# Performance work log

Hardware: AMD Instinct MI355X
Metric: run time of the kernel (lower is better)

Reference implementation:

```python
import jax, jax.numpy as jnp
import numpy as np

# dims
B, T = 2, 256            # batch, seq_len
V, H_CP, R = 512, 2, 2   # vocab, CP horizon, CP rank
E, L, NH, NPOS = 768, 12, 12, 1024  # n_embd, n_layer, n_head, max positions
HD = E // NH             # head dim = 64


def _ln(x, g, b, eps=1e-5):
    m = jnp.mean(x, -1, keepdims=True)
    v = jnp.mean((x - m) ** 2, -1, keepdims=True)
    return (x - m) * jax.lax.rsqrt(v + eps) * g + b


def setup_inputs() -> dict:
    key = jax.random.key(0)
    ks = jax.random.split(key, 10)
    s = 0.02  # GPT2 init std
    n = lambda k, sh: s * jax.random.normal(k, sh, jnp.float32)
    return {
        "input_ids": jax.random.randint(ks[0], (B, T), 0, V, dtype=jnp.int32),
        "wte": n(ks[1], (V, E)),
        "wpe": n(ks[2], (NPOS, E)),
        "ln1_g": jnp.ones((L, E), jnp.float32), "ln1_b": jnp.zeros((L, E), jnp.float32),
        "ln2_g": jnp.ones((L, E), jnp.float32), "ln2_b": jnp.zeros((L, E), jnp.float32),
        "w_qkv": n(ks[3], (L, E, 3 * E)), "b_qkv": jnp.zeros((L, 3 * E), jnp.float32),
        "w_ao": n(ks[4], (L, E, E)), "b_ao": jnp.zeros((L, E), jnp.float32),
        "w_fc": n(ks[5], (L, E, 4 * E)), "b_fc": jnp.zeros((L, 4 * E), jnp.float32),
        "w_mo": n(ks[6], (L, 4 * E, E)), "b_mo": jnp.zeros((L, E), jnp.float32),
        "lnf_g": jnp.ones((E,), jnp.float32), "lnf_b": jnp.zeros((E,), jnp.float32),
        "w_cp": n(ks[7], (E, H_CP * V * R)), "b_cp": jnp.zeros((H_CP * V * R,), jnp.float32),
    }


def reference(input_ids, wte, wpe, ln1_g, ln1_b, ln2_g, ln2_b, w_qkv, b_qkv,
              w_ao, b_ao, w_fc, b_fc, w_mo, b_mo, lnf_g, lnf_b, w_cp, b_cp):
    # --- GPT2 transformer body (eval mode: dropout inactive) ---
    h = wte[input_ids] + wpe[:T]                      # (B,T,E)
    causal = jnp.tril(jnp.ones((T, T), bool))
    inv_sqrt_hd = float(1.0 / np.sqrt(HD))

    def block(h, p):
        l1g, l1b, l2g, l2b, wq, bq, wa, ba, wf, bf, wm, bm = p
        x = _ln(h, l1g, l1b)
        qkv = x @ wq + bq                             # (B,T,3E)
        q, k, v = jnp.split(qkv, 3, axis=-1)
        q = q.reshape(B, T, NH, HD).transpose(0, 2, 1, 3)
        k = k.reshape(B, T, NH, HD).transpose(0, 2, 1, 3)
        v = v.reshape(B, T, NH, HD).transpose(0, 2, 1, 3)
        att = jnp.einsum('bhqd,bhkd->bhqk', q, k) * inv_sqrt_hd
        att = jnp.where(causal, att, jnp.float32(-1e9))
        att = jax.nn.softmax(att, axis=-1)
        o = jnp.einsum('bhqk,bhkd->bhqd', att, v).transpose(0, 2, 1, 3).reshape(B, T, E)
        h = h + o @ wa + ba
        x = _ln(h, l2g, l2b)
        h = h + jax.nn.gelu(x @ wf + bf, approximate=True) @ wm + bm  # gelu_new
        return h, None

    h, _ = jax.lax.scan(block, h, (ln1_g, ln1_b, ln2_g, ln2_b, w_qkv, b_qkv,
                                   w_ao, b_ao, w_fc, b_fc, w_mo, b_mo))
    h = _ln(h, lnf_g, lnf_b)                          # last_hidden_state

    # --- CP joint distribution: sum_r outer(f0_r, f1_r), then positivity(exp) ---
    cp = (h.reshape(B * T, E) @ w_cp + b_cp).reshape(B * T, H_CP, V, R)
    scores = jnp.einsum('nir,njr->nij', cp[:, 0], cp[:, 1])  # (B*T, V, V)
    mjd = jnp.exp(scores).reshape(B, T, V, V)[:, :-H_CP].reshape(-1, V, V)

    # --- windowed targets: targets[b,t,h] = input_ids[b, t+1+h] ---
    off = jnp.arange(T - H_CP)[:, None] + 1 + jnp.arange(H_CP)[None, :]
    tgt = input_ids[:, off].reshape(-1, H_CP)         # (B*(T-H), H)

    # --- entropy loss over unnormalized joint: mean(log Z - log p_target) ---
    n = mjd.shape[0]
    p_t = mjd[jnp.arange(n), tgt[:, 0], tgt[:, 1]]
    Z = mjd.sum((1, 2))
    loss = jnp.mean(jnp.log(Z) - jnp.log(p_t))
    return loss
```

## Files before the change

### kernel.cpp

```cpp
#include <hip/hip_runtime.h>

typedef unsigned short u16;
typedef short short8 __attribute__((ext_vector_type(8)));
typedef float f32x4 __attribute__((ext_vector_type(4)));

constexpr int B_  = 2;
constexpr int T_  = 256;
constexpr int V_  = 512;
constexpr int E_  = 768;
constexpr int L_  = 12;
constexpr int NH_ = 12;
constexpr int HD_ = 64;
constexpr int E3_ = 3 * E_;
constexpr int E4_ = 4 * E_;
constexpr int CPD_ = 2048;
constexpr int NTOK_ = B_ * T_;
constexpr int NVALID_ = B_ * (T_ - 2);
constexpr size_t PS_ = (size_t)NTOK_ * E_;
constexpr size_t QS_ = (size_t)NTOK_ * E3_;
constexpr size_t FS_ = (size_t)NTOK_ * E4_;
constexpr size_t CS_ = (size_t)NTOK_ * CPD_;

__device__ __forceinline__ u16 f2b(float f) {
    union { float f; unsigned int u; } c; c.f = f;
    unsigned int r = (c.u + 0x7FFFu + ((c.u >> 16) & 1u)) >> 16; return (u16)r;
}

__global__ __launch_bounds__(256) void ln_res_k(float* __restrict__ h,
    const float* __restrict__ pb, int np,
    const int* __restrict__ ids, const float* __restrict__ wte,
    const float* __restrict__ wpe,
    const float* __restrict__ g, const float* __restrict__ bta,
    u16* __restrict__ out) {
    int n = blockIdx.x;
    int tid = threadIdx.x;
    size_t off = (size_t)n * E_;
    float v0, v1, v2;
    if (np < 0) {
        int t = n % T_;
        int tok = ids[n];
        size_t wo = (size_t)tok * E_, po = (size_t)t * E_;
        v0 = wte[wo + tid]       + wpe[po + tid];
        v1 = wte[wo + tid + 256] + wpe[po + tid + 256];
        v2 = wte[wo + tid + 512] + wpe[po + tid + 512];
        h[off + tid] = v0; h[off + tid + 256] = v1; h[off + tid + 512] = v2;
    } else {
        v0 = h[off + tid]; v1 = h[off + tid + 256]; v2 = h[off + tid + 512];
        for (int j = 0; j < np; j++) {
            const float* p = pb + (size_t)j * PS_ + off;
            v0 += p[tid]; v1 += p[tid + 256]; v2 += p[tid + 512];
        }
        if (np) { h[off + tid] = v0; h[off + tid + 256] = v1; h[off + tid + 512] = v2; }
    }
    __shared__ float red[256];
    red[tid] = v0 + v1 + v2;
    __syncthreads();
    for (int o = 128; o > 0; o >>= 1) { if (tid < o) red[tid] += red[tid + o]; __syncthreads(); }
    float mean = red[0] * (1.0f / E_);
    __syncthreads();
    float d0 = v0 - mean, d1 = v1 - mean, d2 = v2 - mean;
    red[tid] = d0 * d0 + d1 * d1 + d2 * d2;
    __syncthreads();
    for (int o = 128; o > 0; o >>= 1) { if (tid < o) red[tid] += red[tid + o]; __syncthreads(); }
    float rstd = rsqrtf(red[0] * (1.0f / E_) + 1e-5f);
    u16* y = out + off;
    y[tid]       = f2b(d0 * rstd * g[tid]       + bta[tid]);
    y[tid + 256] = f2b(d1 * rstd * g[tid + 256] + bta[tid + 256]);
    y[tid + 512] = f2b(d2 * rstd * g[tid + 512] + bta[tid + 512]);
}

__global__ __launch_bounds__(512) void mgemm_k(const u16* __restrict__ A,
    const float* __restrict__ W, const float* __restrict__ bias,
    float* __restrict__ outP, int K, int KC, int N) {
    __shared__ u16 As[128 * 40];
    __shared__ u16 Bs[128 * 40];
    int tid = threadIdx.x, lane = tid & 63, wid = tid >> 6;
    int ln15 = lane & 15, quad = lane >> 4;
    int col0 = blockIdx.x * 128, row0 = blockIdx.y * 128;
    int kz = blockIdx.z, kbase = kz * KC;
    int ar = tid >> 2, ak = (tid & 3) * 8;
    const u16* Ag = A + (size_t)(row0 + ar) * K + kbase + ak;
    u16* Aw = &As[ar * 40 + ak];
    int bc = tid & 127, kg = (tid >> 7) * 8;
    const float* Wg = W + (size_t)(kbase + kg) * N + col0 + bc;
    u16* Bw = &Bs[bc * 40 + kg];
    int wr = (wid & 3) * 32, wc = (wid >> 2) * 64;

    f32x4 acc[2][4];
#pragma unroll
    for (int mt = 0; mt < 2; mt++)
#pragma unroll
        for (int nt = 0; nt < 4; nt++) acc[mt][nt] = (f32x4){0.f, 0.f, 0.f, 0.f};

    uint4 av = *(const uint4*)Ag;
    float w[8];
#pragma unroll
    for (int i = 0; i < 8; i++) w[i] = Wg[(size_t)i * N];

    for (int k0 = 0; k0 < KC; k0 += 32) {
        uint4 avn = av;
        float wn[8];
#pragma unroll
        for (int i = 0; i < 8; i++) wn[i] = w[i];
        if (k0 + 32 < KC) {
            avn = *(const uint4*)(Ag + k0 + 32);
#pragma unroll
            for (int i = 0; i < 8; i++) wn[i] = Wg[(size_t)(k0 + 32 + i) * N];
        }
        uint4 bv;
        asm("v_cvt_pk_bf16_f32 %0, %1, %2" : "=v"(bv.x) : "v"(w[0]), "v"(w[1]));
        asm("v_cvt_pk_bf16_f32 %0, %1, %2" : "=v"(bv.y) : "v"(w[2]), "v"(w[3]));
        asm("v_cvt_pk_bf16_f32 %0, %1, %2" : "=v"(bv.z) : "v"(w[4]), "v"(w[5]));
        asm("v_cvt_pk_bf16_f32 %0, %1, %2" : "=v"(bv.w) : "v"(w[6]), "v"(w[7]));
        __syncthreads();
        *(uint4*)Aw = av;
        *(uint4*)Bw = bv;
        __syncthreads();
        short8 af[2], bf[4];
#pragma unroll
        for (int mt = 0; mt < 2; mt++)
            af[mt] = *(const short8*)&As[(wr + mt * 16 + ln15) * 40 + quad * 8];
#pragma unroll
        for (int nt = 0; nt < 4; nt++)
            bf[nt] = *(const short8*)&Bs[(wc + nt * 16 + ln15) * 40 + quad * 8];
#pragma unroll
        for (int mt = 0; mt < 2; mt++)
#pragma unroll
            for (int nt = 0; nt < 4; nt++)
                acc[mt][nt] = __builtin_amdgcn_mfma_f32_16x16x32_bf16(
                    af[mt], bf[nt], acc[mt][nt], 0, 0, 0);
        av = avn;
#pragma unroll
        for (int i = 0; i < 8; i++) w[i] = wn[i];
    }
    float* dst = outP + (size_t)kz * NTOK_ * N;
#pragma unroll
    for (int mt = 0; mt < 2; mt++) {
#pragma unroll
        for (int nt = 0; nt < 4; nt++) {
            int c = col0 + wc + nt * 16 + ln15;
            float bb = (kz == 0) ? bias[c] : 0.f;
#pragma unroll
            for (int r = 0; r < 4; r++) {
                int rw = row0 + wr + mt * 16 + quad * 4 + r;
                dst[(size_t)rw * N + c] = acc[mt][nt][r] + bb;
            }
        }
    }
}

__global__ __launch_bounds__(256) void gelu_k(const float* __restrict__ p0,
    const float* __restrict__ p1, u16* __restrict__ out) {
    size_t i = ((size_t)blockIdx.x * 256 + threadIdx.x) * 4;
    float4 a = *(const float4*)&p0[i];
    float4 b = *(const float4*)&p1[i];
    float u[4] = {a.x + b.x, a.y + b.y, a.z + b.z, a.w + b.w};
    ushort4 o;
    u16* op = (u16*)&o;
#pragma unroll
    for (int j = 0; j < 4; j++) {
        float uu = u[j];
        float inner = 0.7978845608028654f * (uu + 0.044715f * uu * uu * uu);
        op[j] = f2b(0.5f * uu * (1.0f + tanhf(inner)));
    }
    *(ushort4*)&out[i] = o;
}

constexpr int KSTR_ = 72;
constexpr int PSTR_ = 264;
__global__ __launch_bounds__(256) void fattn_k(const float* __restrict__ qp,
    u16* __restrict__ o) {
    __shared__ u16 Ks[256 * KSTR_];
    __shared__ u16 Vt[64 * PSTR_];
    __shared__ u16 Ps[64 * PSTR_];
    int qt = blockIdx.x;
    int bh = blockIdx.y;
    int hh = bh % NH_, b = bh / NH_;
    int tid = threadIdx.x, lane = tid & 63, wid = tid >> 6;
    int ln15 = lane & 15, quad = lane >> 4;

    int sr = tid >> 4, sd = (tid & 15) * 4;
#pragma unroll
    for (int pass = 0; pass < 16; pass++) {
        int rr = sr + pass * 16;
        size_t rowbase = (size_t)(b * T_ + rr) * E3_ + hh * HD_ + sd;
        float kx = 0.f, ky = 0.f, kz = 0.f, kw = 0.f;
        float vx = 0.f, vy = 0.f, vz = 0.f, vw = 0.f;
#pragma unroll
        for (int pi = 0; pi < 4; pi++) {
            float4 kk = *(const float4*)&qp[pi * QS_ + rowbase + E_];
            float4 vv = *(const float4*)&qp[pi * QS_ + rowbase + 2 * E_];
            kx += kk.x; ky += kk.y; kz += kk.z; kw += kk.w;
            vx += vv.x; vy += vv.y; vz += vv.z; vw += vv.w;
        }
        uint2 pk;
        asm("v_cvt_pk_bf16_f32 %0, %1, %2" : "=v"(pk.x) : "v"(kx), "v"(ky));
        asm("v_cvt_pk_bf16_f32 %0, %1, %2" : "=v"(pk.y) : "v"(kz), "v"(kw));
        *(uint2*)&Ks[rr * KSTR_ + sd] = pk;
        Vt[(sd + 0) * PSTR_ + rr] = f2b(vx);
        Vt[(sd + 1) * PSTR_ + rr] = f2b(vy);
        Vt[(sd + 2) * PSTR_ + rr] = f2b(vz);
        Vt[(sd + 3) * PSTR_ + rr] = f2b(vw);
    }

    size_t qbase = (size_t)(b * T_ + qt * 64 + wid * 16 + ln15) * E3_ + hh * HD_;
    short8 qf[2];
#pragma unroll
    for (int ks = 0; ks < 2; ks++) {
        float s8[8] = {0.f, 0.f, 0.f, 0.f, 0.f, 0.f, 0.f, 0.f};
#pragma unroll
        for (int pi = 0; pi < 4; pi++) {
            const float* src = &qp[pi * QS_ + qbase + ks * 32 + quad * 8];
            float4 a = *(const float4*)src;
            float4 b4 = *(const float4*)(src + 4);
            s8[0] += a.x; s8[1] += a.y; s8[2] += a.z; s8[3] += a.w;
            s8[4] += b4.x; s8[5] += b4.y; s8[6] += b4.z; s8[7] += b4.w;
        }
        union { short8 s; unsigned int u[4]; } uq;
#pragma unroll
        for (int i = 0; i < 4; i++)
            asm("v_cvt_pk_bf16_f32 %0, %1, %2" : "=v"(uq.u[i]) : "v"(s8[2 * i]), "v"(s8[2 * i + 1]));
        qf[ks] = uq.s;
    }

    __syncthreads();

    f32x4 s[16];
#pragma unroll
    for (int nt = 0; nt < 16; nt++) s[nt] = (f32x4){0.f, 0.f, 0.f, 0.f};
#pragma unroll
    for (int ks = 0; ks < 2; ks++) {
#pragma unroll
        for (int nt = 0; nt < 16; nt++) {
            short8 kf = *(const short8*)&Ks[(nt * 16 + ln15) * KSTR_ + ks * 32 + quad * 8];
            s[nt] = __builtin_amdgcn_mfma_f32_16x16x32_bf16(qf[ks], kf, s[nt], 0, 0, 0);
        }
    }

#pragma unroll
    for (int r = 0; r < 4; r++) {
        int q = qt * 64 + wid * 16 + quad * 4 + r;
        float m = -1e30f;
#pragma unroll
        for (int nt = 0; nt < 16; nt++) {
            int j = nt * 16 + ln15;
            float sv = (j <= q) ? s[nt][r] * 0.125f : -1e9f;
            s[nt][r] = sv;
            m = fmaxf(m, sv);
        }
        m = fmaxf(m, __shfl_xor(m, 1));
        m = fmaxf(m, __shfl_xor(m, 2));
        m = fmaxf(m, __shfl_xor(m, 4));
        m = fmaxf(m, __shfl_xor(m, 8));
        float sum = 0.f;
#pragma unroll
        for (int nt = 0; nt < 16; nt++) {
            float p = __expf(s[nt][r] - m);
            s[nt][r] = p;
            sum += p;
        }
        sum += __shfl_xor(sum, 1);
        sum += __shfl_xor(sum, 2);
        sum += __shfl_xor(sum, 4);
        sum += __shfl_xor(sum, 8);
        float inv = 1.0f / sum;
#pragma unroll
        for (int nt = 0; nt < 16; nt++) s[nt][r] *= inv;
    }

#pragma unroll
    for (int nt = 0; nt < 16; nt++)
#pragma unroll
        for (int r = 0; r < 4; r++)
            Ps[(wid * 16 + quad * 4 + r) * PSTR_ + nt * 16 + ln15] = f2b(s[nt][r]);

    __syncthreads();

    f32x4 oacc[4];
#pragma unroll
    for (int dt = 0; dt < 4; dt++) oacc[dt] = (f32x4){0.f, 0.f, 0.f, 0.f};
#pragma unroll
    for (int ks = 0; ks < 8; ks++) {
        short8 pf = *(const short8*)&Ps[(wid * 16 + ln15) * PSTR_ + ks * 32 + quad * 8];
#pragma unroll
        for (int dt = 0; dt < 4; dt++) {
            short8 vf = *(const short8*)&Vt[(dt * 16 + ln15) * PSTR_ + ks * 32 + quad * 8];
            oacc[dt] = __builtin_amdgcn_mfma_f32_16x16x32_bf16(pf, vf, oacc[dt], 0, 0, 0);
        }
    }

#pragma unroll
    for (int dt = 0; dt < 4; dt++) {
#pragma unroll
        for (int r = 0; r < 4; r++) {
            int q = qt * 64 + wid * 16 + quad * 4 + r;
            o[(size_t)(b * T_ + q) * E_ + hh * HD_ + dt * 16 + ln15] = f2b(oacc[dt][r]);
        }
    }
}

__global__ __launch_bounds__(256) void zloss_k(const float* __restrict__ cp,
    const int* __restrict__ ids, float* __restrict__ lossv) {
    int n = blockIdx.x;
    int b = n / (T_ - 2), t = n % (T_ - 2);
    int nf = b * T_ + t;
    size_t base = (size_t)nf * CPD_;
    __shared__ float A0[V_], A1[V_], B0[V_], B1[V_];
    __shared__ float red[256];
    int tid = threadIdx.x;
    for (int v = tid; v < V_; v += 256) {
        float a0 = 0.f, a1 = 0.f, b0 = 0.f, b1 = 0.f;
#pragma unroll
        for (int pi = 0; pi < 4; pi++) {
            const float* ap = cp + pi * CS_ + base;
            float2 av = *(const float2*)&ap[2 * v];
            float2 bv = *(const float2*)&ap[1024 + 2 * v];
            a0 += av.x; a1 += av.y; b0 += bv.x; b1 += bv.y;
        }
        A0[v] = a0; A1[v] = a1; B0[v] = b0; B1[v] = b1;
    }
    __syncthreads();
    float acc = 0.f;
    for (int j = tid; j < V_; j += 256) {
        float b0 = B0[j], b1 = B1[j];
        for (int i = 0; i < V_; i++)
            acc += __expf(A0[i] * b0 + A1[i] * b1);
    }
    red[tid] = acc; __syncthreads();
    for (int off = 128; off > 0; off >>= 1) { if (tid < off) red[tid] += red[tid + off]; __syncthreads(); }
    if (tid == 0) {
        int t0 = ids[b * T_ + t + 1];
        int t1 = ids[b * T_ + t + 2];
        float score = A0[t0] * B0[t1] + A1[t0] * B1[t1];
        lossv[n] = logf(red[0]) - score;
    }
}

__global__ __launch_bounds__(256) void reduce_k(const float* __restrict__ lossv,
    unsigned int* __restrict__ out) {
    __shared__ float red[256];
    int tid = threadIdx.x;
    float s = 0.f;
    for (int i = tid; i < NVALID_; i += 256) s += lossv[i];
    red[tid] = s; __syncthreads();
    for (int off = 128; off > 0; off >>= 1) { if (tid < off) red[tid] += red[tid + off]; __syncthreads(); }
    if (tid == 0) {
        float loss = red[0] / (float)NVALID_;
        union { float f; unsigned int u; } cv; cv.f = loss;
        unsigned int b = (cv.u + 0x7FFFu + ((cv.u >> 16) & 1u)) >> 16;
        out[0] = (b << 16) | b;
    }
}

extern "C" void kernel_launch(void* const* d_in, const int* in_sizes, int n_in,
                              void* d_out, int out_size, void* d_ws, size_t ws_size,
                              hipStream_t stream) {
    const int*   ids  = (const int*)d_in[0];
    const float* wte  = (const float*)d_in[1];
    const float* wpe  = (const float*)d_in[2];
    const float* ln1g = (const float*)d_in[3];
    const float* ln1b = (const float*)d_in[4];
    const float* ln2g = (const float*)d_in[5];
    const float* ln2b = (const float*)d_in[6];
    const float* wqkv = (const float*)d_in[7];
    const float* bqkv = (const float*)d_in[8];
    const float* wao  = (const float*)d_in[9];
    const float* bao  = (const float*)d_in[10];
    const float* wfc  = (const float*)d_in[11];
    const float* bfc  = (const float*)d_in[12];
    const float* wmo  = (const float*)d_in[13];
    const float* bmo  = (const float*)d_in[14];
    const float* lnfg = (const float*)d_in[15];
    const float* lnfb = (const float*)d_in[16];
    const float* wcp  = (const float*)d_in[17];
    const float* bcp  = (const float*)d_in[18];

    char* p = (char*)d_ws;
    float* h    = (float*)p; p += (size_t)NTOK_ * E_ * 4;
    u16*   x    = (u16*)p;   p += (size_t)NTOK_ * E_ * 2;
    u16*   aob  = (u16*)p;   p += (size_t)NTOK_ * E_ * 2;
    u16*   fcb  = (u16*)p;   p += (size_t)NTOK_ * E4_ * 2;
    float* pbuf = (float*)p; p += 4 * QS_ * 4;
    float* lossv = (float*)p; p += 4096;

    for (int l = 0; l < L_; l++) {
        ln_res_k<<<NTOK_, 256, 0, stream>>>(h, pbuf, l ? 8 : -1, ids, wte, wpe,
                                            ln1g + l * E_, ln1b + l * E_, x);
        mgemm_k<<<dim3(E3_ / 128, 4, 4), 512, 0, stream>>>(
            x, wqkv + (size_t)l * E_ * E3_, bqkv + l * E3_, pbuf, E_, 192, E3_);
        fattn_k<<<dim3(4, B_ * NH_), 256, 0, stream>>>(pbuf, aob);
        mgemm_k<<<dim3(E_ / 128, 4, 8), 512, 0, stream>>>(
            aob, wao + (size_t)l * E_ * E_, bao + l * E_, pbuf, E_, 96, E_);
        ln_res_k<<<NTOK_, 256, 0, stream>>>(h, pbuf, 8, ids, wte, wpe,
                                            ln2g + l * E_, ln2b + l * E_, x);
        mgemm_k<<<dim3(E4_ / 128, 4, 2), 512, 0, stream>>>(
            x, wfc + (size_t)l * E_ * E4_, bfc + l * E4_, pbuf, E_, 384, E4_);
        gelu_k<<<(NTOK_ * E4_) / 1024, 256, 0, stream>>>(pbuf, pbuf + FS_, fcb);
        mgemm_k<<<dim3(E_ / 128, 4, 8), 512, 0, stream>>>(
            fcb, wmo + (size_t)l * E4_ * E_, bmo + l * E_, pbuf, E4_, 384, E_);
    }
    ln_res_k<<<NTOK_, 256, 0, stream>>>(h, pbuf, 8, ids, wte, wpe, lnfg, lnfb, x);
    mgemm_k<<<dim3(CPD_ / 128, 4, 4), 512, 0, stream>>>(
        x, wcp, bcp, pbuf, E_, 192, CPD_);
    zloss_k<<<NVALID_, 256, 0, stream>>>(pbuf, ids, lossv);
    reduce_k<<<1, 256, 0, stream>>>(lossv, (unsigned int*)d_out);
}
```

Measured before the change: 1.321 ms.

## Fuse whole forward pass into one cooperative persistent megakernel with grid syncs

After: 4.523 ms. +242.3%, slower.

```diff
diff --git a/kernel.cpp b/kernel.cpp
--- a/kernel.cpp
+++ b/kernel.cpp
@@ -1,4 +1,7 @@
 #include <hip/hip_runtime.h>
+#include <hip/hip_cooperative_groups.h>
+
+namespace cg = cooperative_groups;
 
 typedef unsigned short u16;
 typedef short short8 __attribute__((ext_vector_type(8)));
@@ -25,6 +28,7 @@
     union { float f; unsigned int u; } c; c.f = f;
     unsigned int r = (c.u + 0x7FFFu + ((c.u >> 16) & 1u)) >> 16; return (u16)r;
 }
+
 
 __global__ __launch_bounds__(256) void ln_res_k(float* __restrict__ h,
     const float* __restrict__ pb, int np,
@@ -352,6 +356,406 @@
     }
 }
 
+
+struct MKP {
+    const int* ids; const float* wte; const float* wpe;
+    const float* ln1g; const float* ln1b; const float* ln2g; const float* ln2b;
+    const float* wqkv; const float* bqkv; const float* wao; const float* bao;
+    const float* wfc; const float* bfc; const float* wmo; const float* bmo;
+    const float* lnfg; const float* lnfb; const float* wcp; const float* bcp;
+    float* h; u16* x; u16* aob; u16* fcb; float* pbuf; float* lossv;
+    unsigned int* out;
+};
+
+__device__ void mk_ln_unit(int n, float* h, const float* pb, int np,
+    const int* ids, const float* wte, const float* wpe,
+    const float* g, const float* bta, u16* out, float* red) {
+    int tid = threadIdx.x;
+    size_t off = (size_t)n * E_;
+    float v0 = 0.f, v1 = 0.f, v2 = 0.f;
+    if (tid < 256) {
+        if (np < 0) {
+            int t = n % T_;
+            int tok = ids[n];
+            size_t wo = (size_t)tok * E_, po = (size_t)t * E_;
+            v0 = wte[wo + tid]       + wpe[po + tid];
+            v1 = wte[wo + tid + 256] + wpe[po + tid + 256];
+            v2 = wte[wo + tid + 512] + wpe[po + tid + 512];
+            h[off + tid] = v0; h[off + tid + 256] = v1; h[off + tid + 512] = v2;
+        } else {
+            v0 = h[off + tid]; v1 = h[off + tid + 256]; v2 = h[off + tid + 512];
+            for (int j = 0; j < np; j++) {
+                const float* p = pb + (size_t)j * PS_ + off;
+                v0 += p[tid]; v1 += p[tid + 256]; v2 += p[tid + 512];
+            }
+            if (np) { h[off + tid] = v0; h[off + tid + 256] = v1; h[off + tid + 512] = v2; }
+        }
+        red[tid] = v0 + v1 + v2;
+    }
+    __syncthreads();
+    for (int o = 128; o > 0; o >>= 1) { if (tid < o) red[tid] += red[tid + o]; __syncthreads(); }
+    float mean = red[0] * (1.0f / E_);
+    __syncthreads();
+    float d0 = v0 - mean, d1 = v1 - mean, d2 = v2 - mean;
+    if (tid < 256) red[tid] = d0 * d0 + d1 * d1 + d2 * d2;
+    __syncthreads();
+    for (int o = 128; o > 0; o >>= 1) { if (tid < o) red[tid] += red[tid + o]; __syncthreads(); }
+    float rstd = rsqrtf(red[0] * (1.0f / E_) + 1e-5f);
+    if (tid < 256) {
+        u16* y = out + off;
+        y[tid]       = f2b(d0 * rstd * g[tid]       + bta[tid]);
+        y[tid + 256] = f2b(d1 * rstd * g[tid + 256] + bta[tid + 256]);
+        y[tid + 512] = f2b(d2 * rstd * g[tid + 512] + bta[tid + 512]);
+    }
+    __syncthreads();
+}
+
+__device__ void mk_gemm(const u16* __restrict__ A, const float* __restrict__ W,
+    const float* __restrict__ bias, float* __restrict__ outP,
+    int K, int KC, int N, int ntiles, int nx, u16* As, u16* Bs) {
+    int tid = threadIdx.x, lane = tid & 63, wid = tid >> 6;
+    int ln15 = lane & 15, quad = lane >> 4;
+    int ar = tid >> 2, ak = (tid & 3) * 8;
+    int bc = tid & 127, kg = (tid >> 7) * 8;
+    int wr = (wid & 3) * 32, wc = (wid >> 2) * 64;
+    for (int t = blockIdx.x; t < ntiles; t += 256) {
+        int bx = t % nx, by = (t / nx) & 3, kz = t / (nx * 4);
+        int col0 = bx * 128, row0 = by * 128, kbase = kz * KC;
+        const u16* Ag = A + (size_t)(row0 + ar) * K + kbase + ak;
+        u16* Aw = &As[ar * 40 + ak];
+        const float* Wg = W + (size_t)(kbase + kg) * N + col0 + bc;
+        u16* Bw = &Bs[bc * 40 + kg];
+
+        f32x4 acc[2][4];
+#pragma unroll
+        for (int mt = 0; mt < 2; mt++)
+#pragma unroll
+            for (int nt = 0; nt < 4; nt++) acc[mt][nt] = (f32x4){0.f, 0.f, 0.f, 0.f};
+
+        uint4 av = *(const uint4*)Ag;
+        float w[8];
+#pragma unroll
+        for (int i = 0; i < 8; i++) w[i] = Wg[(size_t)i * N];
+
+        for (int k0 = 0; k0 < KC; k0 += 32) {
+            uint4 avn = av;
+            float wn[8];
+#pragma unroll
+            for (int i = 0; i < 8; i++) wn[i] = w[i];
+            if (k0 + 32 < KC) {
+                avn = *(const uint4*)(Ag + k0 + 32);
+#pragma unroll
+                for (int i = 0; i < 8; i++) wn[i] = Wg[(size_t)(k0 + 32 + i) * N];
+            }
+            uint4 bv;
+            asm("v_cvt_pk_bf16_f32 %0, %1, %2" : "=v"(bv.x) : "v"(w[0]), "v"(w[1]));
+            asm("v_cvt_pk_bf16_f32 %0, %1, %2" : "=v"(bv.y) : "v"(w[2]), "v"(w[3]));
+            asm("v_cvt_pk_bf16_f32 %0, %1, %2" : "=v"(bv.z) : "v"(w[4]), "v"(w[5]));
+            asm("v_cvt_pk_bf16_f32 %0, %1, %2" : "=v"(bv.w) : "v"(w[6]), "v"(w[7]));
+            __syncthreads();
+            *(uint4*)Aw = av;
+            *(uint4*)Bw = bv;
+            __syncthreads();
+            short8 af[2], bf[4];
+#pragma unroll
+            for (int mt = 0; mt < 2; mt++)
+                af[mt] = *(const short8*)&As[(wr + mt * 16 + ln15) * 40 + quad * 8];
+#pragma unroll
+            for (int nt = 0; nt < 4; nt++)
+                bf[nt] = *(const short8*)&Bs[(wc + nt * 16 + ln15) * 40 + quad * 8];
+#pragma unroll
+            for (int mt = 0; mt < 2; mt++)
+#pragma unroll
+                for (int nt = 0; nt < 4; nt++)
+                    acc[mt][nt] = __builtin_amdgcn_mfma_f32_16x16x32_bf16(
+                        af[mt], bf[nt], acc[mt][nt], 0, 0, 0);
+            av = avn;
+#pragma unroll
+            for (int i = 0; i < 8; i++) w[i] = wn[i];
+        }
+        float* dst = outP + (size_t)kz * NTOK_ * N;
+#pragma unroll
+        for (int mt = 0; mt < 2; mt++) {
+#pragma unroll
+            for (int nt = 0; nt < 4; nt++) {
+                int c = col0 + wc + nt * 16 + ln15;
+                float bb = (kz == 0) ? bias[c] : 0.f;
+#pragma unroll
+                for (int r = 0; r < 4; r++) {
+                    int rw = row0 + wr + mt * 16 + quad * 4 + r;
+                    dst[(size_t)rw * N + c] = acc[mt][nt][r] + bb;
+                }
+            }
+        }
+        __syncthreads();
+    }
+}
+
+__device__ void mk_attn_unit(const float* __restrict__ qp, u16* __restrict__ o,
+    int unit, u16* Ks, u16* Vt, u16* Ps) {
+    int qt = unit % 4, bh = unit / 4;
+    int hh = bh % NH_, b = bh / NH_;
+    int tid = threadIdx.x, lane = tid & 63, wid = tid >> 6;
+    int ln15 = lane & 15, quad = lane >> 4;
+
+    int sr = tid >> 4, sd = (tid & 15) * 4;
+#pragma unroll
+    for (int pass = 0; pass < 8; pass++) {
+        int rr = sr + pass * 32;
+        size_t rowbase = (size_t)(b * T_ + rr) * E3_ + hh * HD_ + sd;
+        float kx = 0.f, ky = 0.f, kz = 0.f, kw = 0.f;
+        float vx = 0.f, vy = 0.f, vz = 0.f, vw = 0.f;
+#pragma unroll
+        for (int pi = 0; pi < 4; pi++) {
+            float4 kk = *(const float4*)&qp[pi * QS_ + rowbase + E_];
+            float4 vv = *(const float4*)&qp[pi * QS_ + rowbase + 2 * E_];
+            kx += kk.x; ky += kk.y; kz += kk.z; kw += kk.w;
+            vx += vv.x; vy += vv.y; vz += vv.z; vw += vv.w;
+        }
+        uint2 pk;
+        asm("v_cvt_pk_bf16_f32 %0, %1, %2" : "=v"(pk.x) : "v"(kx), "v"(ky));
+        asm("v_cvt_pk_bf16_f32 %0, %1, %2" : "=v"(pk.y) : "v"(kz), "v"(kw));
+        *(uint2*)&Ks[rr * KSTR_ + sd] = pk;
+        Vt[(sd + 0) * PSTR_ + rr] = f2b(vx);
+        Vt[(sd + 1) * PSTR_ + rr] = f2b(vy);
+        Vt[(sd + 2) * PSTR_ + rr] = f2b(vz);
+        Vt[(sd + 3) * PSTR_ + rr] = f2b(vw);
+    }
+
+    short8 qf[2];
+    f32x4 s[16];
+    if (tid < 256) {
+        size_t qbase = (size_t)(b * T_ + qt * 64 + wid * 16 + ln15) * E3_ + hh * HD_;
+#pragma unroll
+        for (int ks = 0; ks < 2; ks++) {
+            float s8[8] = {0.f, 0.f, 0.f, 0.f, 0.f, 0.f, 0.f, 0.f};
+#pragma unroll
+            for (int pi = 0; pi < 4; pi++) {
+                const float* src = &qp[pi * QS_ + qbase + ks * 32 + quad * 8];
+                float4 a = *(const float4*)src;
+                float4 b4 = *(const float4*)(src + 4);
+                s8[0] += a.x; s8[1] += a.y; s8[2] += a.z; s8[3] += a.w;
+                s8[4] += b4.x; s8[5] += b4.y; s8[6] += b4.z; s8[7] += b4.w;
+            }
+            union { short8 s; unsigned int u[4]; } uq;
+#pragma unroll
+            for (int i = 0; i < 4; i++)
+                asm("v_cvt_pk_bf16_f32 %0, %1, %2" : "=v"(uq.u[i]) : "v"(s8[2 * i]), "v"(s8[2 * i + 1]));
+            qf[ks] = uq.s;
+        }
+    }
+
+    __syncthreads();
+
+    if (tid < 256) {
+#pragma unroll
+        for (int nt = 0; nt < 16; nt++) s[nt] = (f32x4){0.f, 0.f, 0.f, 0.f};
+#pragma unroll
+        for (int ks = 0; ks < 2; ks++) {
+#pragma unroll
+            for (int nt = 0; nt < 16; nt++) {
+                short8 kf = *(const short8*)&Ks[(nt * 16 + ln15) * KSTR_ + ks * 32 + quad * 8];
+                s[nt] = __builtin_amdgcn_mfma_f32_16x16x32_bf16(qf[ks], kf, s[nt], 0, 0, 0);
+            }
+        }
+#pragma unroll
+        for (int r = 0; r < 4; r++) {
+            int q = qt * 64 + wid * 16 + quad * 4 + r;
+            float m = -1e30f;
+#pragma unroll
+            for (int nt = 0; nt < 16; nt++) {
+                int j = nt * 16 + ln15;
+                float sv = (j <= q) ? s[nt][r] * 0.125f : -1e9f;
+                s[nt][r] = sv;
+                m = fmaxf(m, sv);
+            }
+            m = fmaxf(m, __shfl_xor(m, 1));
+            m = fmaxf(m, __shfl_xor(m, 2));
+            m = fmaxf(m, __shfl_xor(m, 4));
+            m = fmaxf(m, __shfl_xor(m, 8));
+            float sum = 0.f;
+#pragma unroll
+            for (int nt = 0; nt < 16; nt++) {
+                float p = __expf(s[nt][r] - m);
+                s[nt][r] = p;
+                sum += p;
+            }
+            sum += __shfl_xor(sum, 1);
+            sum += __shfl_xor(sum, 2);
+            sum += __shfl_xor(sum, 4);
+            sum += __shfl_xor(sum, 8);
+            float inv = 1.0f / sum;
+#pragma unroll
+            for (int nt = 0; nt < 16; nt++) s[nt][r] *= inv;
+        }
+    }
+
+    __syncthreads();
+
+    if (tid < 256) {
+#pragma unroll
+        for (int nt = 0; nt < 16; nt++)
+#pragma unroll
+            for (int r = 0; r < 4; r++)
+                Ps[(wid * 16 + quad * 4 + r) * PSTR_ + nt * 16 + ln15] = f2b(s[nt][r]);
+    }
+
+    __syncthreads();
+
+    if (tid < 256) {
+        f32x4 oacc[4];
+#pragma unroll
+        for (int dt = 0; dt < 4; dt++) oacc[dt] = (f32x4){0.f, 0.f, 0.f, 0.f};
+#pragma unroll
+        for (int ks = 0; ks < 8; ks++) {
+            short8 pf = *(const short8*)&Ps[(wid * 16 + ln15) * PSTR_ + ks * 32 + quad * 8];
+#pragma unroll
+            for (int dt = 0; dt < 4; dt++) {
+                short8 vf = *(const short8*)&Vt[(dt * 16 + ln15) * PSTR_ + ks * 32 + quad * 8];
+                oacc[dt] = __builtin_amdgcn_mfma_f32_16x16x32_bf16(pf, vf, oacc[dt], 0, 0, 0);
+            }
+        }
+#pragma unroll
+        for (int dt = 0; dt < 4; dt++) {
+#pragma unroll
+            for (int r = 0; r < 4; r++) {
+                int q = qt * 64 + wid * 16 + quad * 4 + r;
+                o[(size_t)(b * T_ + q) * E_ + hh * HD_ + dt * 16 + ln15] = f2b(oacc[dt][r]);
+            }
+        }
+    }
+}
+
+__device__ void mk_zloss_unit(const float* cp, const int* ids, float* lossv, int n,
+    float* A0, float* A1, float* B0, float* B1, float* red) {
+    int b = n / (T_ - 2), t = n % (T_ - 2);
+    int nf = b * T_ + t;
+    size_t base = (size_t)nf * CPD_;
+    int tid = threadIdx.x;
+    if (tid < 256) {
+        for (int v = tid; v < V_; v += 256) {
+            float a0 = 0.f, a1 = 0.f, b0 = 0.f, b1 = 0.f;
+#pragma unroll
+            for (int pi = 0; pi < 4; pi++) {
+                const float* ap = cp + pi * CS_ + base;
+                float2 av = *(const float2*)&ap[2 * v];
+                float2 bv = *(const float2*)&ap[1024 + 2 * v];
+                a0 += av.x; a1 += av.y; b0 += bv.x; b1 += bv.y;
+            }
+            A0[v] = a0; A1[v] = a1; B0[v] = b0; B1[v] = b1;
+        }
+    }
+    __syncthreads();
+    float acc = 0.f;
+    if (tid < 256) {
+        for (int j = tid; j < V_; j += 256) {
+            float b0 = B0[j], b1 = B1[j];
+            for (int i = 0; i < V_; i++)
+                acc += __expf(A0[i] * b0 + A1[i] * b1);
+        }
+        red[tid] = acc;
+    }
+    __syncthreads();
+    for (int off = 128; off > 0; off >>= 1) { if (tid < off) red[tid] += red[tid + off]; __syncthreads(); }
+    if (tid == 0) {
+        int t0 = ids[b * T_ + t + 1];
+        int t1 = ids[b * T_ + t + 2];
+        float score = A0[t0] * B0[t1] + A1[t0] * B1[t1];
+        lossv[n] = logf(red[0]) - score;
+    }
+    __syncthreads();
+}
+
+__device__ void mk_reduce(const float* lossv, unsigned int* out, float* red) {
+    int tid = threadIdx.x;
+    if (tid < 256) {
+        float s = 0.f;
+        for (int i = tid; i < NVALID_; i += 256) s += lossv[i];
+        red[tid] = s;
+    }
+    __syncthreads();
+    for (int off = 128; off > 0; off >>= 1) { if (tid < off) red[tid] += red[tid + off]; __syncthreads(); }
+    if (tid == 0) {
+        float loss = red[0] / (float)NVALID_;
+        union { float f; unsigned int u; } cv; cv.f = loss;
+        unsigned int b = (cv.u + 0x7FFFu + ((cv.u >> 16) & 1u)) >> 16;
+        out[0] = (b << 16) | b;
+    }
+}
+
+__global__ __launch_bounds__(512, 2) void mega_k(MKP p) {
+    cg::grid_group grid = cg::this_grid();
+    __shared__ __align__(16) unsigned char smem[70656];
+    u16* As = (u16*)smem;
+    u16* Bs = (u16*)(smem + 10240);
+    u16* Ks = (u16*)smem;
+    u16* Vt = (u16*)(smem + 36864);
+    u16* Ps = Ks;
+    float* red = (float*)smem;
+    float* zA0 = (float*)smem;
+    float* zA1 = zA0 + 512;
+    float* zB0 = zA0 + 1024;
+    float* zB1 = zA0 + 1536;
+    float* zred = zA0 + 2048;
+    int blk = blockIdx.x;
+
+    for (int l = 0; l < L_; l++) {
+        for (int u = blk; u < NTOK_; u += 256)
+            mk_ln_unit(u, p.h, p.pbuf, l ? 8 : -1, p.ids, p.wte, p.wpe,
+                       p.ln1g + l * E_, p.ln1b + l * E_, p.x, red);
+        grid.sync();
+        mk_gemm(p.x, p.wqkv + (size_t)l * E_ * E3_, p.bqkv + l * E3_, p.pbuf,
+                E_, 192, E3_, 288, 18, As, Bs);
+        grid.sync();
+        if (blk < 96) mk_attn_unit(p.pbuf, p.aob, blk, Ks, Vt, Ps);
+        grid.sync();
+        mk_gemm(p.aob, p.wao + (size_t)l * E_ * E_, p.bao + l * E_, p.pbuf,
+                E_, 96, E_, 192, 6, As, Bs);
+        grid.sync();
+        for (int u = blk; u < NTOK_; u += 256)
+            mk_ln_unit(u, p.h, p.pbuf, 8, p.ids, p.wte, p.wpe,
+                       p.ln2g + l * E_, p.ln2b + l * E_, p.x, red);
+        grid.sync();
+        mk_gemm(p.x, p.wfc + (size_t)l * E_ * E4_, p.bfc + l * E4_, p.pbuf,
+                E_, 384, E4_, 192, 24, As, Bs);
+        grid.sync();
+        {
+            const float* p0 = p.pbuf;
+            const float* p1 = p.pbuf + FS_;
+            size_t nitems = (size_t)NTOK_ * E4_ / 4;
+            for (size_t it = (size_t)blk * 512 + threadIdx.x; it < nitems; it += (size_t)256 * 512) {
+                size_t i = it * 4;
+                float4 a = *(const float4*)&p0[i];
+                float4 b = *(const float4*)&p1[i];
+                float u4[4] = {a.x + b.x, a.y + b.y, a.z + b.z, a.w + b.w};
+                ushort4 o;
+                u16* op = (u16*)&o;
+#pragma unroll
+                for (int j = 0; j < 4; j++) {
+                    float uu = u4[j];
+                    float inner = 0.7978845608028654f * (uu + 0.044715f * uu * uu * uu);
+                    op[j] = f2b(0.5f * uu * (1.0f + tanhf(inner)));
+                }
+                *(ushort4*)&p.fcb[i] = o;
+            }
+        }
+        grid.sync();
+        mk_gemm(p.fcb, p.wmo + (size_t)l * E4_ * E_, p.bmo + l * E_, p.pbuf,
+                E4_, 384, E_, 192, 6, As, Bs);
+        grid.sync();
+    }
+    for (int u = blk; u < NTOK_; u += 256)
+        mk_ln_unit(u, p.h, p.pbuf, 8, p.ids, p.wte, p.wpe, p.lnfg, p.lnfb, p.x, red);
+    grid.sync();
+    mk_gemm(p.x, p.wcp, p.bcp, p.pbuf, E_, 192, CPD_, 256, 16, As, Bs);
+    grid.sync();
+    for (int u = blk; u < NVALID_; u += 256)
+        mk_zloss_unit(p.pbuf, p.ids, p.lossv, u, zA0, zA1, zB0, zB1, zred);
+    grid.sync();
+    if (blk == 0) mk_reduce(p.lossv, p.out, red);
+}
+
+
 extern "C" void kernel_launch(void* const* d_in, const int* in_sizes, int n_in,
                               void* d_out, int out_size, void* d_ws, size_t ws_size,
                               hipStream_t stream) {
@@ -383,6 +787,21 @@
     float* pbuf = (float*)p; p += 4 * QS_ * 4;
     float* lossv = (float*)p; p += 4096;
 
+    MKP mk;
+    mk.ids = ids; mk.wte = wte; mk.wpe = wpe;
+    mk.ln1g = ln1g; mk.ln1b = ln1b; mk.ln2g = ln2g; mk.ln2b = ln2b;
+    mk.wqkv = wqkv; mk.bqkv = bqkv; mk.wao = wao; mk.bao = bao;
+    mk.wfc = wfc; mk.bfc = bfc; mk.wmo = wmo; mk.bmo = bmo;
+    mk.lnfg = lnfg; mk.lnfb = lnfb; mk.wcp = wcp; mk.bcp = bcp;
+    mk.h = h; mk.x = x; mk.aob = aob; mk.fcb = fcb; mk.pbuf = pbuf;
+    mk.lossv = lossv; mk.out = (unsigned int*)d_out;
+
+    void* kargs[] = { (void*)&mk };
+    hipError_t err = hipLaunchCooperativeKernel((const void*)mega_k,
+        dim3(256), dim3(512), kargs, 0, stream);
+    if (err == hipSuccess) return;
+    (void)hipGetLastError();
+
     for (int l = 0; l < L_; l++) {
         ln_res_k<<<NTOK_, 256, 0, stream>>>(h, pbuf, l ? 8 : -1, ids, wte, wpe,
                                             ln1g + l * E_, ln1b + l * E_, x);
```

## Replace split-K QKV/FC GEMMs with full-K bf16-output GEMM fusing bias and GELU

Applied to the files above, without the earlier changes.

After: 1.235 ms, median of 2. 6.5% less time.

```diff
diff --git a/kernel.cpp b/kernel.cpp
--- a/kernel.cpp
+++ b/kernel.cpp
@@ -18,7 +18,6 @@
 constexpr int NVALID_ = B_ * (T_ - 2);
 constexpr size_t PS_ = (size_t)NTOK_ * E_;
 constexpr size_t QS_ = (size_t)NTOK_ * E3_;
-constexpr size_t FS_ = (size_t)NTOK_ * E4_;
 constexpr size_t CS_ = (size_t)NTOK_ * CPD_;
 
 __device__ __forceinline__ u16 f2b(float f) {
@@ -149,26 +148,94 @@
     }
 }
 
-__global__ __launch_bounds__(256) void gelu_k(const float* __restrict__ p0,
-    const float* __restrict__ p1, u16* __restrict__ out) {
-    size_t i = ((size_t)blockIdx.x * 256 + threadIdx.x) * 4;
-    float4 a = *(const float4*)&p0[i];
-    float4 b = *(const float4*)&p1[i];
-    float u[4] = {a.x + b.x, a.y + b.y, a.z + b.z, a.w + b.w};
-    ushort4 o;
-    u16* op = (u16*)&o;
-#pragma unroll
-    for (int j = 0; j < 4; j++) {
-        float uu = u[j];
-        float inner = 0.7978845608028654f * (uu + 0.044715f * uu * uu * uu);
-        op[j] = f2b(0.5f * uu * (1.0f + tanhf(inner)));
-    }
-    *(ushort4*)&out[i] = o;
+__global__ __launch_bounds__(512) void mgemm64_k(const u16* __restrict__ A,
+    const float* __restrict__ W, const float* __restrict__ bias,
+    u16* __restrict__ outB, int K, int N, int mode) {
+    __shared__ u16 As[128 * 40];
+    __shared__ u16 Bs[64 * 40];
+    int tid = threadIdx.x, lane = tid & 63, wid = tid >> 6;
+    int ln15 = lane & 15, quad = lane >> 4;
+    int col0 = blockIdx.x * 64, row0 = blockIdx.y * 128;
+    int ar = tid >> 2, ak = (tid & 3) * 8;
+    const u16* Ag = A + (size_t)(row0 + ar) * K + ak;
+    u16* Aw = &As[ar * 40 + ak];
+    int bc = tid & 63, kg = (tid >> 6) * 4;
+    const float* Wg = W + (size_t)kg * N + col0 + bc;
+    u16* Bw = &Bs[bc * 40 + kg];
+    int wr = (wid & 3) * 32, wc = (wid >> 2) * 32;
+
+    f32x4 acc[2][2];
+    acc[0][0] = (f32x4){0.f,0.f,0.f,0.f}; acc[0][1] = (f32x4){0.f,0.f,0.f,0.f};
+    acc[1][0] = (f32x4){0.f,0.f,0.f,0.f}; acc[1][1] = (f32x4){0.f,0.f,0.f,0.f};
+
+    uint4 av = *(const uint4*)Ag;
+    float w[4];
+#pragma unroll
+    for (int i = 0; i < 4; i++) w[i] = Wg[(size_t)i * N];
+
+    for (int k0 = 0; k0 < K; k0 += 32) {
+        uint4 avn = av;
+        float wn[4];
+#pragma unroll
+        for (int i = 0; i < 4; i++) wn[i] = w[i];
+        if (k0 + 32 < K) {
+            avn = *(const uint4*)(Ag + k0 + 32);
+#pragma unroll
+            for (int i = 0; i < 4; i++) wn[i] = Wg[(size_t)(k0 + 32 + i) * N];
+        }
+        uint2 bv;
+        asm("v_cvt_pk_bf16_f32 %0, %1, %2" : "=v"(bv.x) : "v"(w[0]), "v"(w[1]));
+        asm("v_cvt_pk_bf16_f32 %0, %1, %2" : "=v"(bv.y) : "v"(w[2]), "v"(w[3]));
+        __syncthreads();
+        *(uint4*)Aw = av;
+        *(uint2*)Bw = bv;
+        __syncthreads();
+        short8 af[2], bf[2];
+#pragma unroll
+        for (int mt = 0; mt < 2; mt++)
+            af[mt] = *(const short8*)&As[(wr + mt * 16 + ln15) * 40 + quad * 8];
+#pragma unroll
+        for (int nt = 0; nt < 2; nt++)
+            bf[nt] = *(const short8*)&Bs[(wc + nt * 16 + ln15) * 40 + quad * 8];
+#pragma unroll
+        for (int mt = 0; mt < 2; mt++)
+#pragma unroll
+            for (int nt = 0; nt < 2; nt++)
+                acc[mt][nt] = __builtin_amdgcn_mfma_f32_16x16x32_bf16(
+                    af[mt], bf[nt], acc[mt][nt], 0, 0, 0);
+        av = avn;
+#pragma unroll
+        for (int i = 0; i < 4; i++) w[i] = wn[i];
+    }
+#pragma unroll
+    for (int mt = 0; mt < 2; mt++) {
+#pragma unroll
+        for (int nt = 0; nt < 2; nt++) {
+            int c = col0 + wc + nt * 16 + ln15;
+            float bb = bias[c];
+            if (mode == 3) {
+#pragma unroll
+                for (int r = 0; r < 4; r++) {
+                    int rw = row0 + wr + mt * 16 + quad * 4 + r;
+                    outB[(size_t)rw * N + c] = f2b(acc[mt][nt][r] + bb);
+                }
+            } else {
+#pragma unroll
+                for (int r = 0; r < 4; r++) {
+                    int rw = row0 + wr + mt * 16 + quad * 4 + r;
+                    float u = acc[mt][nt][r] + bb;
+                    float inner = 0.7978845608028654f * (u + 0.044715f * u * u * u);
+                    float v = 0.5f * u * (1.0f + tanhf(inner));
+                    outB[(size_t)rw * N + c] = f2b(v);
+                }
+            }
+        }
+    }
 }
 
 constexpr int KSTR_ = 72;
 constexpr int PSTR_ = 264;
-__global__ __launch_bounds__(256) void fattn_k(const float* __restrict__ qp,
+__global__ __launch_bounds__(256) void fattn_k(const u16* __restrict__ qkv,
     u16* __restrict__ o) {
     __shared__ u16 Ks[256 * KSTR_];
     __shared__ u16 Vt[64 * PSTR_];
@@ -183,45 +250,20 @@
 #pragma unroll
     for (int pass = 0; pass < 16; pass++) {
         int rr = sr + pass * 16;
-        size_t rowbase = (size_t)(b * T_ + rr) * E3_ + hh * HD_ + sd;
-        float kx = 0.f, ky = 0.f, kz = 0.f, kw = 0.f;
-        float vx = 0.f, vy = 0.f, vz = 0.f, vw = 0.f;
-#pragma unroll
-        for (int pi = 0; pi < 4; pi++) {
-            float4 kk = *(const float4*)&qp[pi * QS_ + rowbase + E_];
-            float4 vv = *(const float4*)&qp[pi * QS_ + rowbase + 2 * E_];
-            kx += kk.x; ky += kk.y; kz += kk.z; kw += kk.w;
-            vx += vv.x; vy += vv.y; vz += vv.z; vw += vv.w;
-        }
-        uint2 pk;
-        asm("v_cvt_pk_bf16_f32 %0, %1, %2" : "=v"(pk.x) : "v"(kx), "v"(ky));
-        asm("v_cvt_pk_bf16_f32 %0, %1, %2" : "=v"(pk.y) : "v"(kz), "v"(kw));
-        *(uint2*)&Ks[rr * KSTR_ + sd] = pk;
-        Vt[(sd + 0) * PSTR_ + rr] = f2b(vx);
-        Vt[(sd + 1) * PSTR_ + rr] = f2b(vy);
-        Vt[(sd + 2) * PSTR_ + rr] = f2b(vz);
-        Vt[(sd + 3) * PSTR_ + rr] = f2b(vw);
-    }
-
-    size_t qbase = (size_t)(b * T_ + qt * 64 + wid * 16 + ln15) * E3_ + hh * HD_;
+        uint2 kv = *(const uint2*)&qkv[(size_t)(b * T_ + rr) * E3_ + E_ + hh * HD_ + sd];
+        *(uint2*)&Ks[rr * KSTR_ + sd] = kv;
+        ushort4 vv = *(const ushort4*)&qkv[(size_t)(b * T_ + rr) * E3_ + 2 * E_ + hh * HD_ + sd];
+        Vt[(sd + 0) * PSTR_ + rr] = vv.x;
+        Vt[(sd + 1) * PSTR_ + rr] = vv.y;
+        Vt[(sd + 2) * PSTR_ + rr] = vv.z;
+        Vt[(sd + 3) * PSTR_ + rr] = vv.w;
+    }
+
+    const u16* Qg = qkv + (size_t)(b * T_ + qt * 64 + wid * 16 + ln15) * E3_ + hh * HD_;
     short8 qf[2];
 #pragma unroll
-    for (int ks = 0; ks < 2; ks++) {
-        float s8[8] = {0.f, 0.f, 0.f, 0.f, 0.f, 0.f, 0.f, 0.f};
-#pragma unroll
-        for (int pi = 0; pi < 4; pi++) {
-            const float* src = &qp[pi * QS_ + qbase + ks * 32 + quad * 8];
-            float4 a = *(const float4*)src;
-            float4 b4 = *(const float4*)(src + 4);
-            s8[0] += a.x; s8[1] += a.y; s8[2] += a.z; s8[3] += a.w;
-            s8[4] += b4.x; s8[5] += b4.y; s8[6] += b4.z; s8[7] += b4.w;
-        }
-        union { short8 s; unsigned int u[4]; } uq;
-#pragma unroll
-        for (int i = 0; i < 4; i++)
-            asm("v_cvt_pk_bf16_f32 %0, %1, %2" : "=v"(uq.u[i]) : "v"(s8[2 * i]), "v"(s8[2 * i + 1]));
-        qf[ks] = uq.s;
-    }
+    for (int ks = 0; ks < 2; ks++)
+        qf[ks] = *(const short8*)&Qg[ks * 32 + quad * 8];
 
     __syncthreads();
 
@@ -380,22 +422,22 @@
     u16*   x    = (u16*)p;   p += (size_t)NTOK_ * E_ * 2;
     u16*   aob  = (u16*)p;   p += (size_t)NTOK_ * E_ * 2;
     u16*   fcb  = (u16*)p;   p += (size_t)NTOK_ * E4_ * 2;
+    u16*   qkvB = (u16*)p;   p += (size_t)NTOK_ * E3_ * 2;
     float* pbuf = (float*)p; p += 4 * QS_ * 4;
     float* lossv = (float*)p; p += 4096;
 
     for (int l = 0; l < L_; l++) {
         ln_res_k<<<NTOK_, 256, 0, stream>>>(h, pbuf, l ? 8 : -1, ids, wte, wpe,
                                             ln1g + l * E_, ln1b + l * E_, x);
-        mgemm_k<<<dim3(E3_ / 128, 4, 4), 512, 0, stream>>>(
-            x, wqkv + (size_t)l * E_ * E3_, bqkv + l * E3_, pbuf, E_, 192, E3_);
-        fattn_k<<<dim3(4, B_ * NH_), 256, 0, stream>>>(pbuf, aob);
+        mgemm64_k<<<dim3(E3_ / 64, 4), 512, 0, stream>>>(
+            x, wqkv + (size_t)l * E_ * E3_, bqkv + l * E3_, qkvB, E_, E3_, 3);
+        fattn_k<<<dim3(4, B_ * NH_), 256, 0, stream>>>(qkvB, aob);
         mgemm_k<<<dim3(E_ / 128, 4, 8), 512, 0, stream>>>(
             aob, wao + (size_t)l * E_ * E_, bao + l * E_, pbuf, E_, 96, E_);
         ln_res_k<<<NTOK_, 256, 0, stream>>>(h, pbuf, 8, ids, wte, wpe,
                                             ln2g + l * E_, ln2b + l * E_, x);
-        mgemm_k<<<dim3(E4_ / 128, 4, 2), 512, 0, stream>>>(
-            x, wfc + (size_t)l * E_ * E4_, bfc + l * E4_, pbuf, E_, 384, E4_);
-        gelu_k<<<(NTOK_ * E4_) / 1024, 256, 0, stream>>>(pbuf, pbuf + FS_, fcb);
+        mgemm64_k<<<dim3(E4_ / 64, 4), 512, 0, stream>>>(
+            x, wfc + (size_t)l * E_ * E4_, bfc + l * E4_, fcb, E_, E4_, 1);
         mgemm_k<<<dim3(E_ / 128, 4, 8), 512, 0, stream>>>(
             fcb, wmo + (size_t)l * E4_ * E_, bmo + l * E_, pbuf, E4_, 384, E_);
     }
```
